# Kernel tuning notes

Measured on AMD Instinct MI355X. Metric: run time of the kernel, lower is better.

## Reference

```python
import jax, jax.numpy as jnp
import numpy as np

HIDDEN = 512
EMBED = 512
VOCAB = 32000
BRANCH = 4
LEVELS = 9  # level 0 = root, level LEVELS-1 = leaves (complete 4-ary tree)
N_NODES = sum(BRANCH ** l for l in range(LEVELS))  # 87381


def setup_inputs() -> dict:
    key = jax.random.key(0)
    ks = jax.random.split(key, 16)
    s = 1.0 / np.sqrt(HIDDEN)
    inp = {
        "token_ids": jax.random.randint(ks[0], (N_NODES,), 0, VOCAB, dtype=jnp.int32),
        "emb": jax.random.normal(ks[1], (VOCAB, EMBED), jnp.float32) * 0.02,
        "Wi": jax.random.normal(ks[2], (EMBED, HIDDEN), jnp.float32) * s,
        "Ui": jax.random.normal(ks[3], (HIDDEN, HIDDEN), jnp.float32) * s,
        "bi": jnp.zeros((HIDDEN,), jnp.float32),
        "Wf": jax.random.normal(ks[4], (EMBED, HIDDEN), jnp.float32) * s,
        "Uf": jax.random.normal(ks[5], (HIDDEN, HIDDEN), jnp.float32) * s,
        "bf": jnp.zeros((HIDDEN,), jnp.float32),
        "Wo": jax.random.normal(ks[6], (EMBED, HIDDEN), jnp.float32) * s,
        "Uo": jax.random.normal(ks[7], (HIDDEN, HIDDEN), jnp.float32) * s,
        "bo": jnp.zeros((HIDDEN,), jnp.float32),
        "Wu": jax.random.normal(ks[8], (EMBED, HIDDEN), jnp.float32) * s,
        "Uu": jax.random.normal(ks[9], (HIDDEN, HIDDEN), jnp.float32) * s,
        "bu": jnp.zeros((HIDDEN,), jnp.float32),
        "branching": BRANCH,
        "n_levels": LEVELS,
    }
    return inp


def reference(token_ids, emb, Wi, Ui, bi, Wf, Uf, bf, Wo, Uo, bo, Wu, Uu, bu,
              branching, n_levels):
    # Level-synchronous Child-Sum Tree-LSTM over a complete `branching`-ary tree.
    # token_ids is laid out level by level, root first.
    B = int(branching)
    L = int(n_levels)
    H = Wi.shape[1]
    level_sizes = [B ** l for l in range(L)]
    offsets = np.concatenate([[0], np.cumsum(level_sizes)])  # static Python ints

    # Leaves: original code sets h = c = 0 (leaf embedding is computed but unused).
    h = jnp.zeros((level_sizes[-1], H), dtype=emb.dtype)
    c = jnp.zeros((level_sizes[-1], H), dtype=emb.dtype)
    hs_levels = [h]  # hidden states collected leaves -> root (level order)

    for l in range(L - 2, -1, -1):
        n = level_sizes[l]
        x = jnp.take(emb, token_ids[offsets[l]:offsets[l + 1]], axis=0)  # [n, E]
        ch_h = h.reshape(n, B, H)  # children of node k are contiguous
        ch_c = c.reshape(n, B, H)
        h_tilde = ch_h.sum(axis=1)  # [n, H] child-sum
        i = jax.nn.sigmoid(x @ Wi + h_tilde @ Ui + bi)
        # per-child forget gates: [n, B, H]
        f = jax.nn.sigmoid((x @ Wf + bf)[:, None, :] + ch_h @ Uf)
        o = jax.nn.sigmoid(x @ Wo + h_tilde @ Uo + bo)
        u = jnp.tanh(x @ Wu + h_tilde @ Uu + bu)
        c = i * u + (f * ch_c).sum(axis=1)
        h = o * jnp.tanh(c)
        hs_levels.append(h)

    hidden_states = jnp.concatenate(hs_levels, axis=0)  # [N_NODES, H]
    return hidden_states, h, c  # h, c are the root states, shape [1, H]
```

## Files before the change

kernel.cpp:

```cpp
#include <hip/hip_runtime.h>

#define DI __device__ __forceinline__

typedef __attribute__((ext_vector_type(8))) __bf16 bf16x8;
typedef __attribute__((ext_vector_type(4))) float f32x4;
typedef __attribute__((ext_vector_type(8))) unsigned short ushort8;
typedef unsigned long long ull;

static DI unsigned short f2b(float f) {
  unsigned int x = __builtin_bit_cast(unsigned int, f);
  unsigned int r = (x + 0x7FFFu + ((x >> 16) & 1u)) >> 16;
  return (unsigned short)r;
}
static DI float b2f(unsigned short u) {
  return __builtin_bit_cast(float, (unsigned int)u << 16);
}
static DI float sigmf(float x) { return 1.0f / (1.0f + __expf(-x)); }

typedef const __attribute__((address_space(1))) void* gcptr;
typedef __attribute__((address_space(3))) void* lptr;
static DI void gl_lds16(const void* g, void* l) {
  __builtin_amdgcn_global_load_lds((gcptr)g, (lptr)l, 16, 0, 0);
}

static DI size_t qaddr(int NT, int row4, int c) {
  int tm = row4 >> 5, tn = c >> 7;
  int rq = row4 & 31, c7 = c & 127;
  int wv = ((rq >> 4) << 1) | (c7 >> 6);
  int mf = (rq >> 2) & 3, nf = (c7 >> 4) & 3;
  int lane = ((rq & 3) << 4) | (c7 & 15);
  return ((size_t)(tm * NT + tn) << 12) + (size_t)((((wv << 4) + (mf << 2) + nf) << 6) + lane);
}

__global__ void prep_pack(const float* __restrict__ Wi, const float* __restrict__ Ui,
                          const float* __restrict__ bi, const float* __restrict__ Wf,
                          const float* __restrict__ Uf, const float* __restrict__ bfv,
                          const float* __restrict__ Wo, const float* __restrict__ Uo,
                          const float* __restrict__ bo, const float* __restrict__ Wu,
                          const float* __restrict__ Uu, const float* __restrict__ bu,
                          unsigned short* __restrict__ Wp, unsigned short* __restrict__ Upiou,
                          unsigned short* __restrict__ Upf, float* __restrict__ bias)
{
  int u = blockIdx.x * blockDim.x + threadIdx.x;
  if (u < 131072) {
    int k8 = u >> 11, n = u & 2047;
    const float* W = (n < 512) ? Wi : (n < 1024) ? Wf : (n < 1536) ? Wo : Wu;
    int c = n & 511;
    ushort8 pk;
    #pragma unroll
    for (int t = 0; t < 8; ++t) pk[t] = f2b(W[(size_t)(k8*8+t)*512 + c]);
    *(ushort8*)&Wp[(size_t)u*8] = pk;
  } else if (u < 131072 + 98304) {
    int v = u - 131072;
    int k8 = v / 1536, n = v - k8*1536;
    const float* U = (n < 512) ? Ui : (n < 1024) ? Uo : Uu;
    int c = n & 511;
    ushort8 pk;
    #pragma unroll
    for (int t = 0; t < 8; ++t) pk[t] = f2b(U[(size_t)(k8*8+t)*512 + c]);
    *(ushort8*)&Upiou[(size_t)v*8] = pk;
  } else {
    int v = u - 229376;
    int k8 = v >> 9, c = v & 511;
    ushort8 pk;
    #pragma unroll
    for (int t = 0; t < 8; ++t) pk[t] = f2b(Uf[(size_t)(k8*8+t)*512 + c]);
    *(ushort8*)&Upf[(size_t)v*8] = pk;
  }
  if (u < 2048) {
    bias[u] = (u < 512) ? bi[u] : (u < 1024) ? bfv[u-512] : (u < 1536) ? bo[u-1024] : bu[u-1536];
  }
}

__global__ void gather_x(const int* __restrict__ tok, const float* __restrict__ emb,
                         unsigned short* __restrict__ X)
{
  int u = blockIdx.x * blockDim.x + threadIdx.x;
  if (u >= 22272*64) return;
  int R = u >> 6, ch = u & 63;
  int l, node;
  if (R < 512)       { l = R >> 7; node = R & 127; int sz = 1 << (2*l); if (node >= sz) node = sz - 1; }
  else if (R < 768)  { l = 4; node = R - 512; }
  else if (R < 1792) { l = 5; node = R - 768; }
  else if (R < 5888) { l = 6; node = R - 1792; }
  else               { l = 7; node = R - 5888; }
  static const int offs_c[8] = {0,1,5,21,85,341,1365,5461};
  int tk = tok[offs_c[l] + node];
  const float* src = emb + (size_t)tk*512 + ch*8;
  ushort8 pk;
  #pragma unroll
  for (int t = 0; t < 8; ++t) pk[t] = f2b(src[t]);
  *(ushort8*)&X[(size_t)u*8] = pk;
}

struct GDesc {
  const unsigned short* A;
  const unsigned short* Bp;
  ull* C;
  int M, N, NT;
};

__global__ __launch_bounds__(256)
void gemm512(GDesc g1, GDesc g2, int split, const float* __restrict__ bias)
{
  __shared__ unsigned short As[2][128*64];
  __shared__ unsigned short Bs[2][8*128*8];

  const int nwg = gridDim.x;
  const int orig = blockIdx.x;
  const int q = nwg >> 3, r = nwg & 7;
  const int xcd = orig & 7, idx = orig >> 3;
  const int wg = (xcd < r ? xcd*(q+1) : r*(q+1) + (xcd - r)*q) + idx;

  const bool role1 = (wg < split);
  GDesc g = role1 ? g1 : g2;
  const int lwg = role1 ? wg : wg - split;
  const int tm = lwg / g.NT, tn = lwg - tm * g.NT;

  const int tid = threadIdx.x;
  const int wave = tid >> 6, lane = tid & 63;
  const int Mbase = tm * 128, Nbase = tn * 128;
  const int wr = wave >> 1, wc = wave & 1;

  const int arow_l = wave*8 + (lane >> 3);
  const int acol8  = lane & 7;
  const int sw8    = arow_l & 7;

  f32x4 acc[4][4] = {};

  auto STAGE = [&](int p, int k0) {
    #pragma unroll
    for (int c = 0; c < 4; ++c) {
      int grow = Mbase + c*32 + arow_l;
      if (grow >= g.M) grow = g.M - 1;
      gl_lds16(g.A + (size_t)grow*512 + k0 + ((acol8 ^ sw8) * 8),
               &As[p][(c*32 + wave*8) * 64]);
    }
    #pragma unroll
    for (int c = 0; c < 4; ++c) {
      int k8 = c*2 + (wave >> 1);
      int colh = (wave & 1) * 64;
      gl_lds16(g.Bp + ((size_t)((k0 >> 3) + k8) * g.N + Nbase + colh + lane) * 8,
               &Bs[p][(k8*128 + colh) * 8]);
    }
  };

  auto COMPUTE = [&](int p) {
    #pragma unroll
    for (int ks = 0; ks < 2; ++ks) {
      bf16x8 af[4], bfr[4];
      #pragma unroll
      for (int mf = 0; mf < 4; ++mf) {
        int row = wr*64 + mf*16 + (lane & 15);
        int kc  = ks*4 + (lane >> 4);
        af[mf] = *(const bf16x8*)&As[p][row*64 + ((kc ^ (row & 7)) * 8)];
      }
      #pragma unroll
      for (int nf = 0; nf < 4; ++nf) {
        int col = wc*64 + nf*16 + (lane & 15);
        int k8  = ks*4 + (lane >> 4);
        bfr[nf] = *(const bf16x8*)&Bs[p][(k8*128 + col) * 8];
      }
      #pragma unroll
      for (int mf = 0; mf < 4; ++mf)
        #pragma unroll
        for (int nf = 0; nf < 4; ++nf)
          acc[mf][nf] = __builtin_amdgcn_mfma_f32_16x16x32_bf16(af[mf], bfr[nf], acc[mf][nf], 0, 0, 0);
    }
  };

  STAGE(0, 0);
  __syncthreads();
  #pragma unroll
  for (int it = 0; it < 7; ++it) {
    STAGE((it + 1) & 1, (it + 1) * 64);
    COMPUTE(it & 1);
    __syncthreads();
  }
  COMPUTE(1);

  float bv[4] = {0.f, 0.f, 0.f, 0.f};
  if (bias != nullptr && role1) {
    #pragma unroll
    for (int nf = 0; nf < 4; ++nf) bv[nf] = bias[Nbase + wc*64 + nf*16 + (lane & 15)];
  }
  ull* Cb = g.C + ((size_t)(tm * g.NT + tn) << 12) + ((size_t)wave << 10);
  #pragma unroll
  for (int mf = 0; mf < 4; ++mf)
    #pragma unroll
    for (int nf = 0; nf < 4; ++nf) {
      f32x4 a = acc[mf][nf];
      ull pk = (ull)f2b(a[0] + bv[nf]) | ((ull)f2b(a[1] + bv[nf]) << 16)
             | ((ull)f2b(a[2] + bv[nf]) << 32) | ((ull)f2b(a[3] + bv[nf]) << 48);
      Cb[(mf*4 + nf)*64 + lane] = pk;
    }
}

__global__ __launch_bounds__(256)
void combine2(const ull* __restrict__ Gq,
              const ull* __restrict__ Rq,
              const ull* __restrict__ Fq,
              const float* __restrict__ cch,
              float* __restrict__ hout,
              unsigned short* __restrict__ hbf,
              float* __restrict__ cout,
              unsigned short* __restrict__ htout,
              float* __restrict__ rootx,
              int n)
{
  const int b = blockIdx.x, t = threadIdx.x;
  #pragma unroll
  for (int half = 0; half < 2; ++half) {
    const int c = t + half * 256;
    ull gi4 = Gq[qaddr(16, b, c)];
    ull gf4 = Gq[qaddr(16, b, c + 512)];
    ull go4 = Gq[qaddr(16, b, c + 1024)];
    ull gu4 = Gq[qaddr(16, b, c + 1536)];
    ull ri4 = 0, ro4 = 0, ru4 = 0;
    if (Rq) {
      ri4 = Rq[qaddr(12, b, c)];
      ro4 = Rq[qaddr(12, b, c + 512)];
      ru4 = Rq[qaddr(12, b, c + 1024)];
    }
    float hts = 0.f;
    #pragma unroll
    for (int rI = 0; rI < 4; ++rI) {
      int j = b*4 + rI;
      float gi = b2f((unsigned short)(gi4 >> (16*rI)));
      float gf = b2f((unsigned short)(gf4 >> (16*rI)));
      float go = b2f((unsigned short)(go4 >> (16*rI)));
      float gu = b2f((unsigned short)(gu4 >> (16*rI)));
      float iv = sigmf(gi + b2f((unsigned short)(ri4 >> (16*rI))));
      float ov = sigmf(go + b2f((unsigned short)(ro4 >> (16*rI))));
      float uv = tanhf(gu + b2f((unsigned short)(ru4 >> (16*rI))));
      float fs = 0.f;
      if (Fq) {
        ull f4 = Fq[qaddr(4, j, c)];
        const float* cc = cch + (size_t)(j*4)*512 + c;
        #pragma unroll
        for (int k = 0; k < 4; ++k)
          fs += sigmf(gf + b2f((unsigned short)(f4 >> (16*k)))) * cc[(size_t)k*512];
      }
      float cv = iv*uv + fs;
      float hv = ov * tanhf(cv);
      if (j < n) {
        hout[(size_t)j*512 + c] = hv;
        hbf[(size_t)j*512 + c]  = f2b(hv);
        cout[(size_t)j*512 + c] = cv;
        if (rootx && j == 0) { rootx[c] = hv; rootx[512 + c] = cv; }
        hts += hv;
      }
    }
    if (htout) htout[(size_t)b*512 + c] = f2b(hts);
  }
}

extern "C" void kernel_launch(void* const* d_in, const int* in_sizes, int n_in,
                              void* d_out, int out_size, void* d_ws, size_t ws_size,
                              hipStream_t stream)
{
  const int*   tok = (const int*)d_in[0];
  const float* emb = (const float*)d_in[1];
  const float* Wi  = (const float*)d_in[2];
  const float* Ui  = (const float*)d_in[3];
  const float* bi  = (const float*)d_in[4];
  const float* Wf  = (const float*)d_in[5];
  const float* Uf  = (const float*)d_in[6];
  const float* bfv = (const float*)d_in[7];
  const float* Wo  = (const float*)d_in[8];
  const float* Uo  = (const float*)d_in[9];
  const float* bo  = (const float*)d_in[10];
  const float* Wu  = (const float*)d_in[11];
  const float* Uu  = (const float*)d_in[12];
  const float* bu  = (const float*)d_in[13];

  char* ws = (char*)d_ws;
  unsigned short* Wp    = (unsigned short*)(ws + 0);
  unsigned short* Upiou = (unsigned short*)(ws + 2097152);
  unsigned short* Upf   = (unsigned short*)(ws + 3670016);
  float*          bias  = (float*)        (ws + 4194304);
  unsigned short* hbf   = (unsigned short*)(ws + 4202496);
  unsigned short* htbf  = (unsigned short*)(ws + 26571776);
  float*          cbuf  = (float*)        (ws + 32163840);
  ull*            RiouQ = (ull*)          (ws + 76902400);
  ull*            RfQ   = (ull*)          (ws + 89485312);

  char* ob = (char*)d_out;
  ull*            Gq = (ull*)ob;
  unsigned short* X  = (unsigned short*)(ob + 91226112);
  float* fout = (float*)d_out;

  static const int  offs[9]    = {0,1,5,21,85,341,1365,5461,21845};
  static const int  padbase[8] = {0,128,256,384,512,768,1792,5888};
  static const long outoff[8]  = {87380,87376,87360,87296,87040,86016,81920,65536};

  prep_pack<<<1024, 256, 0, stream>>>(Wi,Ui,bi,Wf,Uf,bfv,Wo,Uo,bo,Wu,Uu,bu,
                                      Wp,Upiou,Upf,bias);
  gather_x<<<(22272*64)/256, 256, 0, stream>>>(tok, emb, X);

  GDesc gA { X, Wp, Gq, 22272, 2048, 16 };
  gemm512<<<174*16, 256, 0, stream>>>(gA, gA, 174*16, bias);

  combine2<<<4096, 256, 0, stream>>>(Gq + (size_t)padbase[7]*512, nullptr, nullptr, nullptr,
      fout + (size_t)outoff[7]*512, hbf + (size_t)offs[7]*512, cbuf + (size_t)offs[7]*512,
      htbf + (size_t)offs[6]*512, nullptr, 16384);

  for (int l = 6; l >= 0; --l) {
    int n = 1 << (2*l);
    int tm1 = (n + 127) / 128, tm2 = (4*n + 127) / 128;
    int split = tm1 * 12;
    GDesc g1 { htbf + (size_t)offs[l]*512,   Upiou, RiouQ, n,   1536, 12 };
    GDesc g2 { hbf  + (size_t)offs[l+1]*512, Upf,   RfQ,   4*n, 512,  4  };
    gemm512<<<split + tm2*4, 256, 0, stream>>>(g1, g2, split, nullptr);
    combine2<<<(n + 3) / 4, 256, 0, stream>>>(
        Gq + (size_t)padbase[l]*512, RiouQ, RfQ, cbuf + (size_t)offs[l+1]*512,
        fout + (size_t)outoff[l]*512, hbf + (size_t)offs[l]*512, cbuf + (size_t)offs[l]*512,
        (l > 0) ? htbf + (size_t)offs[l-1]*512 : nullptr,
        (l == 0) ? fout + (size_t)87381*512 : nullptr,
        n);
  }

  hipMemsetAsync(d_out, 0, (size_t)65536*512*4, stream);
}
```

Measured before the change: 286.7 us.

## Replace 128x128 GEMM with 256x256 eight-wave pipelined MFMA kernel

```diff
diff --git a/kernel.cpp b/kernel.cpp
--- a/kernel.cpp
+++ b/kernel.cpp
@@ -93,6 +93,14 @@
   *(ushort8*)&X[(size_t)u*8] = pk;
 }
 
+__global__ void fill_zero(f32x4* __restrict__ p, size_t n16)
+{
+  size_t i = (size_t)blockIdx.x * blockDim.x + threadIdx.x;
+  size_t stride = (size_t)gridDim.x * blockDim.x;
+  f32x4 z = {0.f, 0.f, 0.f, 0.f};
+  for (; i < n16; i += stride) p[i] = z;
+}
+
 struct GDesc {
   const unsigned short* A;
   const unsigned short* Bp;
@@ -100,100 +108,114 @@
   int M, N, NT;
 };
 
-__global__ __launch_bounds__(256)
-void gemm512(GDesc g1, GDesc g2, int split, const float* __restrict__ bias)
-{
-  __shared__ unsigned short As[2][128*64];
-  __shared__ unsigned short Bs[2][8*128*8];
-
-  const int nwg = gridDim.x;
-  const int orig = blockIdx.x;
+#define FENCE asm volatile("" ::: "memory")
+#define SBAR  { FENCE; __builtin_amdgcn_s_barrier(); FENCE; }
+#define VMCNT0 asm volatile("s_waitcnt vmcnt(0)" ::: "memory")
+
+__global__ __launch_bounds__(512)
+void gemm8p(GDesc g1, GDesc g2, int split, const float* __restrict__ bias)
+{
+  extern __shared__ unsigned short lds[];
+  constexpr int ASZ = 256*64, BSZ = 8*256*8;
+
+  const int nwg = gridDim.x, orig = blockIdx.x;
   const int q = nwg >> 3, r = nwg & 7;
   const int xcd = orig & 7, idx = orig >> 3;
-  const int wg = (xcd < r ? xcd*(q+1) : r*(q+1) + (xcd - r)*q) + idx;
+  const int wg = (xcd < r ? xcd*(q+1) : r*(q+1) + (xcd-r)*q) + idx;
 
   const bool role1 = (wg < split);
   GDesc g = role1 ? g1 : g2;
   const int lwg = role1 ? wg : wg - split;
-  const int tm = lwg / g.NT, tn = lwg - tm * g.NT;
+  const int TN = g.N >> 8;
+  const int tm = lwg / TN, tn = lwg - tm*TN;
+  const int Mbase = tm << 8, Nbase = tn << 8;
 
   const int tid = threadIdx.x;
   const int wave = tid >> 6, lane = tid & 63;
-  const int Mbase = tm * 128, Nbase = tn * 128;
-  const int wr = wave >> 1, wc = wave & 1;
-
-  const int arow_l = wave*8 + (lane >> 3);
-  const int acol8  = lane & 7;
-  const int sw8    = arow_l & 7;
-
-  f32x4 acc[4][4] = {};
-
-  auto STAGE = [&](int p, int k0) {
-    #pragma unroll
-    for (int c = 0; c < 4; ++c) {
-      int grow = Mbase + c*32 + arow_l;
-      if (grow >= g.M) grow = g.M - 1;
-      gl_lds16(g.A + (size_t)grow*512 + k0 + ((acol8 ^ sw8) * 8),
-               &As[p][(c*32 + wave*8) * 64]);
-    }
-    #pragma unroll
-    for (int c = 0; c < 4; ++c) {
-      int k8 = c*2 + (wave >> 1);
-      int colh = (wave & 1) * 64;
-      gl_lds16(g.Bp + ((size_t)((k0 >> 3) + k8) * g.N + Nbase + colh + lane) * 8,
-               &Bs[p][(k8*128 + colh) * 8]);
+  const int wr = wave >> 2, wc = wave & 3;
+
+  const int lrow8 = lane >> 3;
+  const int schunk = (lane & 7) ^ lrow8;
+
+  f32x4 acc[8][4] = {};
+  bf16x8 bfr[4][2];
+
+  auto STAGE = [&](int t1, int p) {
+    unsigned short* An = lds + p*ASZ;
+    unsigned short* Bn = lds + 2*ASZ + p*BSZ;
+    #pragma unroll
+    for (int i = 0; i < 4; ++i) {
+      int lrow = i*64 + wave*8 + lrow8;
+      int grow = Mbase + lrow; if (grow >= g.M) grow = g.M - 1;
+      gl_lds16(g.A + (size_t)grow*512 + t1*64 + schunk*8,
+               An + (i*64 + wave*8)*64);
+    }
+    #pragma unroll
+    for (int i = 0; i < 4; ++i) {
+      int k8 = i*2 + (wave >> 2);
+      int colb = (wave & 3)*64;
+      gl_lds16(g.Bp + ((size_t)(t1*8 + k8)*g.N + Nbase + colb + lane)*8,
+               Bn + (k8*256 + colb)*8);
     }
   };
 
-  auto COMPUTE = [&](int p) {
-    #pragma unroll
-    for (int ks = 0; ks < 2; ++ks) {
-      bf16x8 af[4], bfr[4];
-      #pragma unroll
-      for (int mf = 0; mf < 4; ++mf) {
-        int row = wr*64 + mf*16 + (lane & 15);
-        int kc  = ks*4 + (lane >> 4);
-        af[mf] = *(const bf16x8*)&As[p][row*64 + ((kc ^ (row & 7)) * 8)];
-      }
-      #pragma unroll
-      for (int nf = 0; nf < 4; ++nf) {
-        int col = wc*64 + nf*16 + (lane & 15);
-        int k8  = ks*4 + (lane >> 4);
-        bfr[nf] = *(const bf16x8*)&Bs[p][(k8*128 + col) * 8];
-      }
-      #pragma unroll
-      for (int mf = 0; mf < 4; ++mf)
-        #pragma unroll
-        for (int nf = 0; nf < 4; ++nf)
-          acc[mf][nf] = __builtin_amdgcn_mfma_f32_16x16x32_bf16(af[mf], bfr[nf], acc[mf][nf], 0, 0, 0);
-    }
-  };
+  #define RDAF(MQ) { const unsigned short* Ab = lds + p*ASZ;                         \
+    _Pragma("unroll") for (int m = 0; m < 2; ++m) {                                  \
+      int row = wr*128 + ((MQ)*2+m)*16 + (lane & 15);                                \
+      _Pragma("unroll") for (int ks = 0; ks < 2; ++ks) {                             \
+        int kc = ks*4 + (lane >> 4);                                                 \
+        af[m][ks] = *(const bf16x8*)&Ab[row*64 + ((kc ^ (row & 7)) * 8)];            \
+      } } }
+  #define RDBF() { const unsigned short* Bb = lds + 2*ASZ + p*BSZ;                   \
+    _Pragma("unroll") for (int nf = 0; nf < 4; ++nf)                                 \
+      _Pragma("unroll") for (int ks = 0; ks < 2; ++ks) {                             \
+        int k8 = ks*4 + (lane >> 4);                                                 \
+        bfr[nf][ks] = *(const bf16x8*)&Bb[(k8*256 + wc*64 + nf*16 + (lane & 15))*8]; \
+      } }
+  #define MMQ(MQ) { __builtin_amdgcn_s_setprio(1);                                   \
+    _Pragma("unroll") for (int ks = 0; ks < 2; ++ks)                                 \
+      _Pragma("unroll") for (int m = 0; m < 2; ++m)                                  \
+        _Pragma("unroll") for (int nf = 0; nf < 4; ++nf)                             \
+          acc[(MQ)*2+m][nf] = __builtin_amdgcn_mfma_f32_16x16x32_bf16(               \
+              af[m][ks], bfr[nf][ks], acc[(MQ)*2+m][nf], 0, 0, 0);                   \
+    __builtin_amdgcn_s_setprio(0); }
 
   STAGE(0, 0);
-  __syncthreads();
+  VMCNT0;
+  SBAR;
+  for (int t = 0; t < 8; ++t) {
+    const int p = t & 1;
+    bf16x8 af[2][2];
+    RDBF(); RDAF(0);
+    if (t < 7) STAGE(t+1, p^1);
+    SBAR;
+    MMQ(0);
+    SBAR;
+    RDAF(1); SBAR; MMQ(1); SBAR;
+    RDAF(2); SBAR; MMQ(2); SBAR;
+    RDAF(3);
+    SBAR;
+    MMQ(3);
+    VMCNT0;
+    SBAR;
+  }
+
+  float bv[4];
   #pragma unroll
-  for (int it = 0; it < 7; ++it) {
-    STAGE((it + 1) & 1, (it + 1) * 64);
-    COMPUTE(it & 1);
-    __syncthreads();
-  }
-  COMPUTE(1);
-
-  float bv[4] = {0.f, 0.f, 0.f, 0.f};
-  if (bias != nullptr && role1) {
-    #pragma unroll
-    for (int nf = 0; nf < 4; ++nf) bv[nf] = bias[Nbase + wc*64 + nf*16 + (lane & 15)];
-  }
-  ull* Cb = g.C + ((size_t)(tm * g.NT + tn) << 12) + ((size_t)wave << 10);
+  for (int nf = 0; nf < 4; ++nf)
+    bv[nf] = (bias != nullptr && role1) ? bias[Nbase + wc*64 + nf*16 + (lane & 15)] : 0.f;
   #pragma unroll
-  for (int mf = 0; mf < 4; ++mf)
+  for (int mf = 0; mf < 8; ++mf) {
+    int row4 = ((Mbase + wr*128 + mf*16) >> 2) + (lane >> 4);
     #pragma unroll
     for (int nf = 0; nf < 4; ++nf) {
+      int col = Nbase + wc*64 + nf*16 + (lane & 15);
       f32x4 a = acc[mf][nf];
       ull pk = (ull)f2b(a[0] + bv[nf]) | ((ull)f2b(a[1] + bv[nf]) << 16)
              | ((ull)f2b(a[2] + bv[nf]) << 32) | ((ull)f2b(a[3] + bv[nf]) << 48);
-      Cb[(mf*4 + nf)*64 + lane] = pk;
-    }
+      g.C[qaddr(g.NT, row4, col)] = pk;
+    }
+  }
 }
 
 __global__ __launch_bounds__(256)
@@ -299,7 +321,7 @@
   gather_x<<<(22272*64)/256, 256, 0, stream>>>(tok, emb, X);
 
   GDesc gA { X, Wp, Gq, 22272, 2048, 16 };
-  gemm512<<<174*16, 256, 0, stream>>>(gA, gA, 174*16, bias);
+  gemm8p<<<87*8, 512, 131072, stream>>>(gA, gA, 87*8, bias);
 
   combine2<<<4096, 256, 0, stream>>>(Gq + (size_t)padbase[7]*512, nullptr, nullptr, nullptr,
       fout + (size_t)outoff[7]*512, hbf + (size_t)offs[7]*512, cbuf + (size_t)offs[7]*512,
@@ -307,11 +329,11 @@
 
   for (int l = 6; l >= 0; --l) {
     int n = 1 << (2*l);
-    int tm1 = (n + 127) / 128, tm2 = (4*n + 127) / 128;
-    int split = tm1 * 12;
+    int tm1 = (n + 255) / 256, tm2 = (4*n + 255) / 256;
+    int split = tm1 * 6;
     GDesc g1 { htbf + (size_t)offs[l]*512,   Upiou, RiouQ, n,   1536, 12 };
     GDesc g2 { hbf  + (size_t)offs[l+1]*512, Upf,   RfQ,   4*n, 512,  4  };
-    gemm512<<<split + tm2*4, 256, 0, stream>>>(g1, g2, split, nullptr);
+    gemm8p<<<split + tm2*2, 512, 131072, stream>>>(g1, g2, split, nullptr);
     combine2<<<(n + 3) / 4, 256, 0, stream>>>(
         Gq + (size_t)padbase[l]*512, RiouQ, RfQ, cbuf + (size_t)offs[l+1]*512,
         fout + (size_t)outoff[l]*512, hbf + (size_t)offs[l]*512, cbuf + (size_t)offs[l]*512,
@@ -320,5 +342,5 @@
         n);
   }
 
-  hipMemsetAsync(d_out, 0, (size_t)65536*512*4, stream);
-}
+  fill_zero<<<2048, 256, 0, stream>>>((f32x4*)d_out, (size_t)65536*512*4/16);
+}
```

Result: slower. 323.2 us (+12.7%).

## Fuse level-7 gate epilogue and leaf zeroing into input-projection GEMM

Applied to the files above, without the earlier changes.

```diff
diff --git a/kernel.cpp b/kernel.cpp
--- a/kernel.cpp
+++ b/kernel.cpp
@@ -22,6 +22,8 @@
 static DI void gl_lds16(const void* g, void* l) {
   __builtin_amdgcn_global_load_lds((gcptr)g, (lptr)l, 16, 0, 0);
 }
+
+#define GCOL(g, d) ((((d) >> 5) << 7) + ((g) << 5) + ((d) & 31))
 
 static DI size_t qaddr(int NT, int row4, int c) {
   int tm = row4 >> 5, tn = c >> 7;
@@ -44,11 +46,12 @@
   int u = blockIdx.x * blockDim.x + threadIdx.x;
   if (u < 131072) {
     int k8 = u >> 11, n = u & 2047;
-    const float* W = (n < 512) ? Wi : (n < 1024) ? Wf : (n < 1536) ? Wo : Wu;
-    int c = n & 511;
+    int gate = (n >> 5) & 3;
+    int d = ((n >> 7) << 5) | (n & 31);
+    const float* W = (gate == 0) ? Wi : (gate == 1) ? Wf : (gate == 2) ? Wo : Wu;
     ushort8 pk;
     #pragma unroll
-    for (int t = 0; t < 8; ++t) pk[t] = f2b(W[(size_t)(k8*8+t)*512 + c]);
+    for (int t = 0; t < 8; ++t) pk[t] = f2b(W[(size_t)(k8*8+t)*512 + d]);
     *(ushort8*)&Wp[(size_t)u*8] = pk;
   } else if (u < 131072 + 98304) {
     int v = u - 131072;
@@ -68,7 +71,9 @@
     *(ushort8*)&Upf[(size_t)v*8] = pk;
   }
   if (u < 2048) {
-    bias[u] = (u < 512) ? bi[u] : (u < 1024) ? bfv[u-512] : (u < 1536) ? bo[u-1024] : bu[u-1536];
+    int gate = (u >> 5) & 3;
+    int d = ((u >> 7) << 5) | (u & 31);
+    bias[u] = (gate == 0) ? bi[d] : (gate == 1) ? bfv[d] : (gate == 2) ? bo[d] : bu[d];
   }
 }
 
@@ -99,18 +104,23 @@
   ull* C;
   int M, N, NT;
 };
-
+struct L7P {
+  float* hout; unsigned short* hb; float* cb; unsigned short* ht;
+  float* zbase; size_t z4;
+};
+
+template<bool FUSED>
 __global__ __launch_bounds__(256)
-void gemm512(GDesc g1, GDesc g2, int split, const float* __restrict__ bias)
-{
-  __shared__ unsigned short As[2][128*64];
-  __shared__ unsigned short Bs[2][8*128*8];
-
-  const int nwg = gridDim.x;
-  const int orig = blockIdx.x;
+void gemm512(GDesc g1, GDesc g2, int split, const float* __restrict__ bias, L7P l7)
+{
+  __shared__ float smemf[128*132];
+  unsigned short* As = (unsigned short*)smemf;
+  unsigned short* Bs = (unsigned short*)smemf + 2*128*64;
+
+  const int nwg = gridDim.x, orig = blockIdx.x;
   const int q = nwg >> 3, r = nwg & 7;
   const int xcd = orig & 7, idx = orig >> 3;
-  const int wg = (xcd < r ? xcd*(q+1) : r*(q+1) + (xcd - r)*q) + idx;
+  const int wg = (xcd < r ? xcd*(q+1) : r*(q+1) + (xcd-r)*q) + idx;
 
   const bool role1 = (wg < split);
   GDesc g = role1 ? g1 : g2;
@@ -134,14 +144,14 @@
       int grow = Mbase + c*32 + arow_l;
       if (grow >= g.M) grow = g.M - 1;
       gl_lds16(g.A + (size_t)grow*512 + k0 + ((acol8 ^ sw8) * 8),
-               &As[p][(c*32 + wave*8) * 64]);
+               As + p*(128*64) + (c*32 + wave*8)*64);
     }
     #pragma unroll
     for (int c = 0; c < 4; ++c) {
       int k8 = c*2 + (wave >> 1);
       int colh = (wave & 1) * 64;
       gl_lds16(g.Bp + ((size_t)((k0 >> 3) + k8) * g.N + Nbase + colh + lane) * 8,
-               &Bs[p][(k8*128 + colh) * 8]);
+               Bs + p*(8*128*8) + (k8*128 + colh)*8);
     }
   };
 
@@ -153,13 +163,13 @@
       for (int mf = 0; mf < 4; ++mf) {
         int row = wr*64 + mf*16 + (lane & 15);
         int kc  = ks*4 + (lane >> 4);
-        af[mf] = *(const bf16x8*)&As[p][row*64 + ((kc ^ (row & 7)) * 8)];
+        af[mf] = *(const bf16x8*)&As[p*(128*64) + row*64 + ((kc ^ (row & 7)) * 8)];
       }
       #pragma unroll
       for (int nf = 0; nf < 4; ++nf) {
         int col = wc*64 + nf*16 + (lane & 15);
         int k8  = ks*4 + (lane >> 4);
-        bfr[nf] = *(const bf16x8*)&Bs[p][(k8*128 + col) * 8];
+        bfr[nf] = *(const bf16x8*)&Bs[p*(8*128*8) + (k8*128 + col) * 8];
       }
       #pragma unroll
       for (int mf = 0; mf < 4; ++mf)
@@ -179,21 +189,77 @@
   }
   COMPUTE(1);
 
-  float bv[4] = {0.f, 0.f, 0.f, 0.f};
-  if (bias != nullptr && role1) {
-    #pragma unroll
-    for (int nf = 0; nf < 4; ++nf) bv[nf] = bias[Nbase + wc*64 + nf*16 + (lane & 15)];
-  }
-  ull* Cb = g.C + ((size_t)(tm * g.NT + tn) << 12) + ((size_t)wave << 10);
-  #pragma unroll
-  for (int mf = 0; mf < 4; ++mf)
-    #pragma unroll
-    for (int nf = 0; nf < 4; ++nf) {
-      f32x4 a = acc[mf][nf];
-      ull pk = (ull)f2b(a[0] + bv[nf]) | ((ull)f2b(a[1] + bv[nf]) << 16)
-             | ((ull)f2b(a[2] + bv[nf]) << 32) | ((ull)f2b(a[3] + bv[nf]) << 48);
-      Cb[(mf*4 + nf)*64 + lane] = pk;
-    }
+  auto ZERO_DUTY = [&]() {
+    if constexpr (FUSED) {
+      size_t b4 = (size_t)orig * 3072;
+      f32x4 z = {0.f, 0.f, 0.f, 0.f};
+      f32x4* zp = (f32x4*)l7.zbase;
+      #pragma unroll
+      for (int i = 0; i < 12; ++i) {
+        size_t off = b4 + (size_t)i*256 + tid;
+        if (off < l7.z4) zp[off] = z;
+      }
+    }
+  };
+
+  if (FUSED && tm >= 46) {
+    __syncthreads();
+    #pragma unroll
+    for (int mf = 0; mf < 4; ++mf) {
+      int rbase = wr*64 + mf*16 + (lane >> 4)*4;
+      #pragma unroll
+      for (int nf = 0; nf < 4; ++nf) {
+        int col = wc*64 + nf*16 + (lane & 15);
+        #pragma unroll
+        for (int rr = 0; rr < 4; ++rr)
+          smemf[(rbase + rr)*132 + col] = acc[mf][nf][rr];
+      }
+    }
+    __syncthreads();
+    ZERO_DUTY();
+    const int dlow = tid & 31, rowg = tid >> 5;
+    const int d = tn*32 + dlow;
+    const float bi_ = bias[tn*128      + dlow];
+    const float bo_ = bias[tn*128 + 64 + dlow];
+    const float bu_ = bias[tn*128 + 96 + dlow];
+    const int nodebase = Mbase - 5888 + rowg*16;
+    float hts = 0.f;
+    #pragma unroll
+    for (int rr = 0; rr < 16; ++rr) {
+      int lrow = rowg*16 + rr;
+      float gi = smemf[lrow*132      + dlow];
+      float go = smemf[lrow*132 + 64 + dlow];
+      float gu = smemf[lrow*132 + 96 + dlow];
+      float iv = sigmf(gi + bi_), ov = sigmf(go + bo_), uv = tanhf(gu + bu_);
+      float cv = iv * uv;
+      float hv = ov * tanhf(cv);
+      size_t node = nodebase + rr;
+      l7.hout[node*512 + d] = hv;
+      l7.hb[node*512 + d]   = f2b(hv);
+      l7.cb[node*512 + d]   = cv;
+      hts += hv;
+      if ((rr & 3) == 3) {
+        l7.ht[(size_t)((nodebase + rr - 3) >> 2)*512 + d] = f2b(hts);
+        hts = 0.f;
+      }
+    }
+  } else {
+    ZERO_DUTY();
+    float bv[4];
+    #pragma unroll
+    for (int nf = 0; nf < 4; ++nf)
+      bv[nf] = (bias != nullptr && role1) ? bias[Nbase + wc*64 + nf*16 + (lane & 15)] : 0.f;
+    ull* Cb = g.C + ((size_t)(tm * g.NT + tn) << 12) + ((size_t)wave << 10);
+    #pragma unroll
+    for (int mf = 0; mf < 4; ++mf)
+      #pragma unroll
+      for (int nf = 0; nf < 4; ++nf) {
+        f32x4 a = acc[mf][nf];
+        ull pk = (ull)f2b(a[0] + bv[nf]) | ((ull)f2b(a[1] + bv[nf]) << 16)
+               | ((ull)f2b(a[2] + bv[nf]) << 32) | ((ull)f2b(a[3] + bv[nf]) << 48);
+        Cb[(mf*4 + nf)*64 + lane] = pk;
+      }
+  }
 }
 
 __global__ __launch_bounds__(256)
@@ -212,16 +278,13 @@
   #pragma unroll
   for (int half = 0; half < 2; ++half) {
     const int c = t + half * 256;
-    ull gi4 = Gq[qaddr(16, b, c)];
-    ull gf4 = Gq[qaddr(16, b, c + 512)];
-    ull go4 = Gq[qaddr(16, b, c + 1024)];
-    ull gu4 = Gq[qaddr(16, b, c + 1536)];
-    ull ri4 = 0, ro4 = 0, ru4 = 0;
-    if (Rq) {
-      ri4 = Rq[qaddr(12, b, c)];
-      ro4 = Rq[qaddr(12, b, c + 512)];
-      ru4 = Rq[qaddr(12, b, c + 1024)];
-    }
+    ull gi4 = Gq[qaddr(16, b, GCOL(0, c))];
+    ull gf4 = Gq[qaddr(16, b, GCOL(1, c))];
+    ull go4 = Gq[qaddr(16, b, GCOL(2, c))];
+    ull gu4 = Gq[qaddr(16, b, GCOL(3, c))];
+    ull ri4 = Rq[qaddr(12, b, c)];
+    ull ro4 = Rq[qaddr(12, b, c + 512)];
+    ull ru4 = Rq[qaddr(12, b, c + 1024)];
     float hts = 0.f;
     #pragma unroll
     for (int rI = 0; rI < 4; ++rI) {
@@ -233,14 +296,12 @@
       float iv = sigmf(gi + b2f((unsigned short)(ri4 >> (16*rI))));
       float ov = sigmf(go + b2f((unsigned short)(ro4 >> (16*rI))));
       float uv = tanhf(gu + b2f((unsigned short)(ru4 >> (16*rI))));
+      ull f4 = Fq[qaddr(4, j, c)];
+      const float* cc = cch + (size_t)(j*4)*512 + c;
       float fs = 0.f;
-      if (Fq) {
-        ull f4 = Fq[qaddr(4, j, c)];
-        const float* cc = cch + (size_t)(j*4)*512 + c;
-        #pragma unroll
-        for (int k = 0; k < 4; ++k)
-          fs += sigmf(gf + b2f((unsigned short)(f4 >> (16*k)))) * cc[(size_t)k*512];
-      }
+      #pragma unroll
+      for (int k = 0; k < 4; ++k)
+        fs += sigmf(gf + b2f((unsigned short)(f4 >> (16*k)))) * cc[(size_t)k*512];
       float cv = iv*uv + fs;
       float hv = ov * tanhf(cv);
       if (j < n) {
@@ -284,10 +345,9 @@
   float*          cbuf  = (float*)        (ws + 32163840);
   ull*            RiouQ = (ull*)          (ws + 76902400);
   ull*            RfQ   = (ull*)          (ws + 89485312);
-
-  char* ob = (char*)d_out;
-  ull*            Gq = (ull*)ob;
-  unsigned short* X  = (unsigned short*)(ob + 91226112);
+  ull*            Gq    = (ull*)          (ws + 106262528);
+  unsigned short* X     = (unsigned short*)(ws + 130379776);
+
   float* fout = (float*)d_out;
 
   static const int  offs[9]    = {0,1,5,21,85,341,1365,5461,21845};
@@ -299,19 +359,19 @@
   gather_x<<<(22272*64)/256, 256, 0, stream>>>(tok, emb, X);
 
   GDesc gA { X, Wp, Gq, 22272, 2048, 16 };
-  gemm512<<<174*16, 256, 0, stream>>>(gA, gA, 174*16, bias);
-
-  combine2<<<4096, 256, 0, stream>>>(Gq + (size_t)padbase[7]*512, nullptr, nullptr, nullptr,
-      fout + (size_t)outoff[7]*512, hbf + (size_t)offs[7]*512, cbuf + (size_t)offs[7]*512,
-      htbf + (size_t)offs[6]*512, nullptr, 16384);
-
+  L7P l7 { fout + (size_t)outoff[7]*512, hbf + (size_t)offs[7]*512,
+           cbuf + (size_t)offs[7]*512, htbf + (size_t)offs[6]*512,
+           fout, (size_t)65536*512/4 };
+  gemm512<true><<<174*16, 256, 0, stream>>>(gA, gA, 174*16, bias, l7);
+
+  L7P l7n {};
   for (int l = 6; l >= 0; --l) {
     int n = 1 << (2*l);
     int tm1 = (n + 127) / 128, tm2 = (4*n + 127) / 128;
     int split = tm1 * 12;
     GDesc g1 { htbf + (size_t)offs[l]*512,   Upiou, RiouQ, n,   1536, 12 };
     GDesc g2 { hbf  + (size_t)offs[l+1]*512, Upf,   RfQ,   4*n, 512,  4  };
-    gemm512<<<split + tm2*4, 256, 0, stream>>>(g1, g2, split, nullptr);
+    gemm512<false><<<split + tm2*4, 256, 0, stream>>>(g1, g2, split, nullptr, l7n);
     combine2<<<(n + 3) / 4, 256, 0, stream>>>(
         Gq + (size_t)padbase[l]*512, RiouQ, RfQ, cbuf + (size_t)offs[l+1]*512,
         fout + (size_t)outoff[l]*512, hbf + (size_t)offs[l]*512, cbuf + (size_t)offs[l]*512,
@@ -319,6 +379,4 @@
         (l == 0) ? fout + (size_t)87381*512 : nullptr,
         n);
   }
-
-  hipMemsetAsync(d_out, 0, (size_t)65536*512*4, stream);
-}
+}
```

After: 259.7 us. 9.4% less time.
